# Performance work log

Hardware: AMD Instinct MI355X
Metric: run time of the kernel (lower is better)

Reference implementation:

```python
import jax, jax.numpy as jnp
import numpy as np

NEG_SLOPE = 0.2  # PyG GATConv default


def gat_layer(x, src, dst, W, att_src, att_dst, bias, num_nodes):
    """One PyG-style GATConv (concat=True, add_self_loops handled by caller).
    x: [N, F_in], W: [F_in, H*C], att_src/att_dst: [H, C], bias: [H*C].
    """
    H, C = att_src.shape
    h = (x @ W).reshape(num_nodes, H, C)              # [N, H, C]
    a_src = (h * att_src).sum(-1)                     # [N, H]
    a_dst = (h * att_dst).sum(-1)                     # [N, H]
    e = jax.nn.leaky_relu(a_src[src] + a_dst[dst], NEG_SLOPE)  # [E, H]
    # segment softmax over destination neighborhoods
    m = jax.ops.segment_max(e, dst, num_segments=num_nodes)   # [N, H]
    ex = jnp.exp(e - m[dst])
    denom = jax.ops.segment_sum(ex, dst, num_segments=num_nodes)
    alpha = ex / denom[dst]                           # [E, H]
    out = jax.ops.segment_sum(alpha[:, :, None] * h[src], dst,
                              num_segments=num_nodes)  # [N, H, C]
    return out.reshape(num_nodes, H * C) + bias


def setup_inputs() -> dict:
    key = jax.random.key(0)
    ks = jax.random.split(key, 12)
    N, E, D, H = 50000, 800000, 128, 8
    C = D // H
    x = jax.random.normal(ks[0], (N, D), dtype=jnp.float32)
    edge_index = jax.random.randint(ks[1], (2, E), 0, N, dtype=jnp.int64)
    s = 0.1
    return {
        "x": x,
        "edge_index": edge_index,
        "W1": s * jax.random.normal(ks[2], (D, H * C), dtype=jnp.float32),
        "as1": s * jax.random.normal(ks[3], (H, C), dtype=jnp.float32),
        "ad1": s * jax.random.normal(ks[4], (H, C), dtype=jnp.float32),
        "b1": jnp.zeros((H * C,), dtype=jnp.float32),
        "W2": s * jax.random.normal(ks[5], (D, H * C), dtype=jnp.float32),
        "as2": s * jax.random.normal(ks[6], (H, C), dtype=jnp.float32),
        "ad2": s * jax.random.normal(ks[7], (H, C), dtype=jnp.float32),
        "b2": jnp.zeros((H * C,), dtype=jnp.float32),
    }


def reference(x, edge_index, W1, as1, ad1, b1, W2, as2, ad2, b2):
    n = x.shape[0]
    # PyG GATConv default add_self_loops=True
    loop = jnp.arange(n, dtype=edge_index.dtype)
    src = jnp.concatenate([edge_index[0], loop])
    dst = jnp.concatenate([edge_index[1], loop])
    h = jax.nn.relu(gat_layer(x, src, dst, W1, as1, ad1, b1, n))
    # dropout p=0.5 is identity in eval mode
    return gat_layer(h, src, dst, W2, as2, ad2, b2, n)
```

## Files before the change

kernel.cpp:

```cpp
#include <hip/hip_runtime.h>
#include <math.h>

#define D 128
#define H 8
#define C 16
#define NEG_SLOPE 0.2f
#define SCAN_TILE 1024

typedef unsigned short ushortT;
typedef __attribute__((ext_vector_type(8))) short short8;
typedef __attribute__((ext_vector_type(4))) float f32x4;

__device__ __forceinline__ float bf2f(unsigned short v) {
    union { unsigned int i; float f; } c;
    c.i = ((unsigned int)v) << 16;
    return c.f;
}
__device__ __forceinline__ unsigned short f2bf(float f) {
    union { float f; unsigned int i; } c;
    c.f = f;
    unsigned int lsb = (c.i >> 16) & 1u;
    c.i += 0x7fffu + lsb;
    return (unsigned short)(c.i >> 16);
}

__device__ __forceinline__ int padc(int c) { return (c + 4) & ~3; }



__device__ __forceinline__ void hist_part(
    int tid, const int* __restrict__ ei, int* cursor, int* __restrict__ rank,
    int E) {
    int i4 = tid * 4;
    if (((E & 3) == 0) && i4 + 3 < E) {
        int4 dv = *(const int4*)(ei + (size_t)E + i4);
        int4 r;
        r.x = atomicAdd(cursor + dv.x, 1);
        r.y = atomicAdd(cursor + dv.y, 1);
        r.z = atomicAdd(cursor + dv.z, 1);
        r.w = atomicAdd(cursor + dv.w, 1);
        *(int4*)(rank + i4) = r;
    } else {
        for (int k = i4; k < E && k < i4 + 4; k++)
            rank[k] = atomicAdd(cursor + ei[(size_t)E + k], 1);
    }
}

__device__ __forceinline__ void wprep_part(
    int b2, int t, const float* __restrict__ W1, const float* __restrict__ as1,
    const float* __restrict__ ad1, const float* __restrict__ W2,
    const float* __restrict__ as2, const float* __restrict__ ad2,
    ushortT* __restrict__ wf1_hi, ushortT* __restrict__ wf1_lo,
    ushortT* __restrict__ wf2_hi, ushortT* __restrict__ wf2_lo) {
    const float *W, *att_s, *att_d;
    ushortT *whi, *wlo;
    int idx;
    if (b2 < 9) {
        W = W1; att_s = as1; att_d = ad1; whi = wf1_hi; wlo = wf1_lo;
        idx = b2 * 256 + t;
    } else {
        W = W2; att_s = as2; att_d = ad2; whi = wf2_hi; wlo = wf2_lo;
        idx = (b2 - 9) * 256 + t;
    }
    if (idx >= 4 * 9 * 64) return;
    int lane = idx & 63;
    int nt = (idx >> 6) % 9;
    int kt = idx / (9 * 64);
    int quad = lane >> 4, ncol = lane & 15;
#pragma unroll
    for (int j = 0; j < 8; j++) {
        int k = kt * 32 + quad * 8 + j;
        float v;
        if (nt < 8) {
            v = W[k * D + nt * 16 + ncol];
        } else {
            const float* att = (ncol < 8) ? att_s : att_d;
            int hd = ncol & 7;
            float s = 0.f;
            for (int c = 0; c < 16; c++)
                s += W[k * D + hd * 16 + c] * att[hd * 16 + c];
            v = s;
        }
        unsigned short hi = f2bf(v);
        unsigned short lo = f2bf(v - bf2f(hi));
        whi[idx * 8 + j] = hi;
        wlo[idx * 8 + j] = lo;
    }
}

__device__ __forceinline__ void xsplit_part(
    int idx, const float* __restrict__ x, ushortT* __restrict__ xh,
    ushortT* __restrict__ xl, int n, int nt16) {
    int r = idx >> 4;
    if (r >= nt16 * 16) return;
    int kb = idx & 15;
    float4 v0 = make_float4(0.f, 0.f, 0.f, 0.f), v1 = v0;
    if (r < n) {
        v0 = ((const float4*)(x + (size_t)r * D + kb * 8))[0];
        v1 = ((const float4*)(x + (size_t)r * D + kb * 8))[1];
    }
    int wt = r >> 4, m = r & 15, kt = kb >> 2, quad = kb & 3;
    int base = ((wt * 4 + kt) * 64 + (m + 16 * quad)) * 8;
    ushort4 h0, l0, h1, l1;
    h0.x = f2bf(v0.x); l0.x = f2bf(v0.x - bf2f(h0.x));
    h0.y = f2bf(v0.y); l0.y = f2bf(v0.y - bf2f(h0.y));
    h0.z = f2bf(v0.z); l0.z = f2bf(v0.z - bf2f(h0.z));
    h0.w = f2bf(v0.w); l0.w = f2bf(v0.w - bf2f(h0.w));
    h1.x = f2bf(v1.x); l1.x = f2bf(v1.x - bf2f(h1.x));
    h1.y = f2bf(v1.y); l1.y = f2bf(v1.y - bf2f(h1.y));
    h1.z = f2bf(v1.z); l1.z = f2bf(v1.z - bf2f(h1.z));
    h1.w = f2bf(v1.w); l1.w = f2bf(v1.w - bf2f(h1.w));
    *(ushort4*)(xh + base) = h0;
    *(ushort4*)(xh + base + 4) = h1;
    *(ushort4*)(xl + base) = l0;
    *(ushort4*)(xl + base + 4) = l1;
}

__global__ __launch_bounds__(256) void k_prep(
    const int* __restrict__ ei, int* cursor, int* __restrict__ rank, int E,
    const float* __restrict__ x, ushortT* __restrict__ xh,
    ushortT* __restrict__ xl, int n, int nt16,
    const float* __restrict__ W1, const float* __restrict__ as1,
    const float* __restrict__ ad1, const float* __restrict__ W2,
    const float* __restrict__ as2, const float* __restrict__ ad2,
    ushortT* __restrict__ wf1_hi, ushortT* __restrict__ wf1_lo,
    ushortT* __restrict__ wf2_hi, ushortT* __restrict__ wf2_lo, int nbh) {
    int b = blockIdx.x;
    int t = threadIdx.x;
    if (b < nbh) {
        hist_part(b * 256 + t, ei, cursor, rank, E);
    } else if (b < nbh + 18) {
        wprep_part(b - nbh, t, W1, as1, ad1, W2, as2, ad2,
                   wf1_hi, wf1_lo, wf2_hi, wf2_lo);
    } else {
        xsplit_part((b - nbh - 18) * 256 + t, x, xh, xl, n, nt16);
    }
}


__global__ __launch_bounds__(256) void k_scan_lb(
    const int* __restrict__ cursor, int* __restrict__ poffs,
    int* __restrict__ sstate, int* __restrict__ csrsrc, int n) {
    __shared__ int lds[256];
    __shared__ int bprefix;
    int t = threadIdx.x;
    int b = blockIdx.x;
    int base = b * SCAN_TILE + t * 4;
    int c[4] = {0, 0, 0, 0};
    if (base + 3 < n) {
        int4 q = *(const int4*)(cursor + base);
        c[0] = q.x; c[1] = q.y; c[2] = q.z; c[3] = q.w;
    } else {
        for (int k = 0; k < 4; k++)
            if (base + k < n) c[k] = cursor[base + k];
    }
    int s = padc(c[0]) + padc(c[1]) + padc(c[2]) + padc(c[3]);
    lds[t] = s;
    __syncthreads();
    for (int st = 1; st < 256; st <<= 1) {
        int add = (t >= st) ? lds[t - st] : 0;
        __syncthreads();
        lds[t] += add;
        __syncthreads();
    }
    if (t == 0)
        __hip_atomic_store(&sstate[b], lds[255] | (1 << 30),
                           __ATOMIC_RELEASE, __HIP_MEMORY_SCOPE_AGENT);
    if (t < 64) {
        int v = 0;
        if (t < b) {
            int x;
            do {
                x = __hip_atomic_load(&sstate[t], __ATOMIC_RELAXED,
                                      __HIP_MEMORY_SCOPE_AGENT);
            } while (!(x & (1 << 30)));
            v = x & 0x3FFFFFFF;
        }
#pragma unroll
        for (int o = 32; o > 0; o >>= 1) v += __shfl_down(v, o);
        if (t == 0) bprefix = v;
    }
    __syncthreads();
    int run = bprefix + ((t == 0) ? 0 : lds[t - 1]);
    if (b == 0 && t == 0) poffs[0] = 0;
#pragma unroll
    for (int k = 0; k < 4; k++) {
        int i = base + k;
        if (i < n) {
            int pv = padc(c[k]);
            csrsrc[run + c[k]] = i;
            for (int k2 = c[k] + 1; k2 < pv; k2++)
                csrsrc[run + k2] = n;
            run += pv;
            poffs[i + 1] = run;
        }
    }
}


__device__ __forceinline__ void gemm_wave(
    int wt, int lane, const ushortT* __restrict__ xh,
    const ushortT* __restrict__ xl, const ushortT* __restrict__ wf_hi,
    const ushortT* __restrict__ wf_lo, ushortT* __restrict__ hout,
    float* __restrict__ as_, float* __restrict__ ad_, int n) {
    f32x4 acc[9];
#pragma unroll
    for (int nt = 0; nt < 9; nt++) acc[nt] = (f32x4){0.f, 0.f, 0.f, 0.f};

#pragma unroll
    for (int kt = 0; kt < 4; kt++) {
        short8 a_hi = *(const short8*)(xh + (size_t)((wt * 4 + kt) * 64 + lane) * 8);
        short8 a_lo = *(const short8*)(xl + (size_t)((wt * 4 + kt) * 64 + lane) * 8);
        const ushortT* bh = wf_hi + (size_t)(kt * 576 + lane) * 8;
        const ushortT* bl = wf_lo + (size_t)(kt * 576 + lane) * 8;
#pragma unroll
        for (int nt = 0; nt < 9; nt++) {
            short8 b_hi = *(const short8*)(bh + nt * 512);
            short8 b_lo = *(const short8*)(bl + nt * 512);
            acc[nt] = __builtin_amdgcn_mfma_f32_16x16x32_bf16(a_hi, b_hi, acc[nt], 0, 0, 0);
            acc[nt] = __builtin_amdgcn_mfma_f32_16x16x32_bf16(a_lo, b_hi, acc[nt], 0, 0, 0);
            acc[nt] = __builtin_amdgcn_mfma_f32_16x16x32_bf16(a_hi, b_lo, acc[nt], 0, 0, 0);
        }
    }

    int q = lane >> 4, ncol = lane & 15;
    int rbase = wt * 16 + q * 4;
#pragma unroll
    for (int nt = 0; nt < 8; nt++) {
#pragma unroll
        for (int reg = 0; reg < 4; reg++) {
            int r = rbase + reg;
            if (r < n) hout[(size_t)r * D + nt * 16 + ncol] = f2bf(acc[nt][reg]);
        }
    }
#pragma unroll
    for (int reg = 0; reg < 4; reg++) {
        int r = rbase + reg;
        if (r < n) {
            float v = acc[8][reg];
            if (ncol < 8) as_[r * H + ncol] = v;
            else          ad_[r * H + (ncol - 8)] = v;
        }
    }
}


__global__ __launch_bounds__(256) void k_fillgemm(
    const int* __restrict__ ei, const int* __restrict__ poffs,
    const int* __restrict__ rank, int* __restrict__ csrsrc,
    ushortT* __restrict__ hbuf_s, float* __restrict__ asrc_s, int E,
    const ushortT* __restrict__ xh, const ushortT* __restrict__ xl,
    const ushortT* __restrict__ wf_hi, const ushortT* __restrict__ wf_lo,
    ushortT* __restrict__ hout, float* __restrict__ as_,
    float* __restrict__ ad_, int n, int gb) {
    int b = blockIdx.x;
    int t = threadIdx.x;
    if (b < gb) {
        int wt = b * 4 + (t >> 6);
        if (wt * 16 < n)
            gemm_wave(wt, t & 63, xh, xl, wf_hi, wf_lo, hout, as_, ad_, n);
        return;
    }
    int tid = (b - gb) * 256 + t;
    int E4 = (E + 3) >> 2;
    if (tid < E4) {
        int i4 = tid * 4;
        if (((E & 3) == 0) && i4 + 3 < E) {
            int4 sv = *(const int4*)(ei + i4);
            int4 dv = *(const int4*)(ei + (size_t)E + i4);
            int4 rv = *(const int4*)(rank + i4);
            csrsrc[poffs[dv.x] + rv.x] = sv.x;
            csrsrc[poffs[dv.y] + rv.y] = sv.y;
            csrsrc[poffs[dv.z] + rv.z] = sv.z;
            csrsrc[poffs[dv.w] + rv.w] = sv.w;
        } else {
            for (int k = i4; k < E && k < i4 + 4; k++)
                csrsrc[poffs[ei[(size_t)E + k]] + rank[k]] = ei[k];
        }
    } else if (tid == E4) {
        int total = poffs[n];
        for (int k = 0; k < 8; k++) csrsrc[total + k] = n;
        for (int k = 0; k < D; k++) hbuf_s[(size_t)n * D + k] = 0;
        for (int h = 0; h < H; h++) asrc_s[n * H + h] = -1e30f;
    }
}


__global__ __launch_bounds__(256) void k_gemm_att(
    const ushortT* __restrict__ xh, const ushortT* __restrict__ xl,
    const ushortT* __restrict__ wf_hi, const ushortT* __restrict__ wf_lo,
    ushortT* __restrict__ hout, float* __restrict__ as_,
    float* __restrict__ ad_, int n) {
    int t = threadIdx.x;
    int wt = blockIdx.x * 4 + (t >> 6);
    if (wt * 16 >= n) return;
    gemm_wave(wt, t & 63, xh, xl, wf_hi, wf_lo, hout, as_, ad_, n);
}


__global__ __launch_bounds__(256) void k_aggregate(
    const ushortT* __restrict__ hbuf, const float* __restrict__ asrc,
    const float* __restrict__ adst, const int* __restrict__ csr,
    const int* __restrict__ poffs, const float* __restrict__ bias,
    float* __restrict__ out, ushortT* __restrict__ oh, ushortT* __restrict__ ol,
    int out_mode, int n) {
    int t = threadIdx.x;
    int d = blockIdx.x * 8 + (t >> 5);
    if (d >= n) return;
    int ll = t & 31;
    int h = ll >> 2;

    int off = poffs[d];
    int degp = poffs[d + 1] - off;
    float adh = adst[d * H + h];

    float4 acc0 = make_float4(0.f, 0.f, 0.f, 0.f);
    float4 acc1 = make_float4(0.f, 0.f, 0.f, 0.f);
    float ssum = 0.f;

    int s0 = csr[off + 0], s1 = csr[off + 1], s2 = csr[off + 2], s3 = csr[off + 3];
    for (int j = 0; j < degp; j += 4) {
        int p0 = csr[off + j + 4], p1 = csr[off + j + 5];
        int p2 = csr[off + j + 6], p3 = csr[off + j + 7];
        float e0 = asrc[s0 * H + h] + adh;
        float e1 = asrc[s1 * H + h] + adh;
        float e2 = asrc[s2 * H + h] + adh;
        float e3 = asrc[s3 * H + h] + adh;
        ushort4 u0 = *(const ushort4*)(hbuf + (size_t)s0 * D + ll * 4);
        ushort4 u1 = *(const ushort4*)(hbuf + (size_t)s1 * D + ll * 4);
        ushort4 u2 = *(const ushort4*)(hbuf + (size_t)s2 * D + ll * 4);
        ushort4 u3 = *(const ushort4*)(hbuf + (size_t)s3 * D + ll * 4);
        float w0 = __expf(e0 > 0.f ? e0 : NEG_SLOPE * e0);
        float w1 = __expf(e1 > 0.f ? e1 : NEG_SLOPE * e1);
        float w2 = __expf(e2 > 0.f ? e2 : NEG_SLOPE * e2);
        float w3 = __expf(e3 > 0.f ? e3 : NEG_SLOPE * e3);
        ssum += (w0 + w1) + (w2 + w3);
        acc0.x += w0 * bf2f(u0.x); acc0.y += w0 * bf2f(u0.y);
        acc0.z += w0 * bf2f(u0.z); acc0.w += w0 * bf2f(u0.w);
        acc1.x += w1 * bf2f(u1.x); acc1.y += w1 * bf2f(u1.y);
        acc1.z += w1 * bf2f(u1.z); acc1.w += w1 * bf2f(u1.w);
        acc0.x += w2 * bf2f(u2.x); acc0.y += w2 * bf2f(u2.y);
        acc0.z += w2 * bf2f(u2.z); acc0.w += w2 * bf2f(u2.w);
        acc1.x += w3 * bf2f(u3.x); acc1.y += w3 * bf2f(u3.y);
        acc1.z += w3 * bf2f(u3.z); acc1.w += w3 * bf2f(u3.w);
        s0 = p0; s1 = p1; s2 = p2; s3 = p3;
    }

    float inv = 1.f / ssum;
    float4 b = ((const float4*)bias)[ll];
    float4 r;
    r.x = (acc0.x + acc1.x) * inv + b.x;
    r.y = (acc0.y + acc1.y) * inv + b.y;
    r.z = (acc0.z + acc1.z) * inv + b.z;
    r.w = (acc0.w + acc1.w) * inv + b.w;

    if (out_mode == 0) {
        ((float4*)(out + (size_t)d * D))[ll] = r;
    } else {
        r.x = fmaxf(r.x, 0.f);
        r.y = fmaxf(r.y, 0.f);
        r.z = fmaxf(r.z, 0.f);
        r.w = fmaxf(r.w, 0.f);
        int wt = d >> 4, m = d & 15;
        int kt = ll >> 3, quad = (ll >> 1) & 3, j0 = (ll & 1) * 4;
        int base = ((wt * 4 + kt) * 64 + (m + 16 * quad)) * 8 + j0;
        ushort4 hv, lv;
        hv.x = f2bf(r.x); lv.x = f2bf(r.x - bf2f(hv.x));
        hv.y = f2bf(r.y); lv.y = f2bf(r.y - bf2f(hv.y));
        hv.z = f2bf(r.z); lv.z = f2bf(r.z - bf2f(hv.z));
        hv.w = f2bf(r.w); lv.w = f2bf(r.w - bf2f(hv.w));
        *(ushort4*)(oh + base) = hv;
        *(ushort4*)(ol + base) = lv;
    }
}


extern "C" void kernel_launch(void* const* d_in, const int* in_sizes, int n_in,
                              void* d_out, int out_size, void* d_ws, size_t ws_size,
                              hipStream_t stream) {
    const float* x   = (const float*)d_in[0];
    const int*   ei  = (const int*)d_in[1];
    const float* W1  = (const float*)d_in[2];
    const float* as1 = (const float*)d_in[3];
    const float* ad1 = (const float*)d_in[4];
    const float* b1  = (const float*)d_in[5];
    const float* W2  = (const float*)d_in[6];
    const float* as2 = (const float*)d_in[7];
    const float* ad2 = (const float*)d_in[8];
    const float* b2  = (const float*)d_in[9];
    float* out = (float*)d_out;

    int N = in_sizes[0] / D;
    int E = in_sizes[1] / 2;
    int NT16 = (N + 15) / 16;
    int nb_scan = (N + SCAN_TILE - 1) / SCAN_TILE;
    const int WFN = 4 * 9 * 64 * 8;
    size_t XS = (size_t)NT16 * 2048;
    int E4 = (E + 3) >> 2;

    ushortT* hbuf = (ushortT*)d_ws;
    ushortT* xsh  = hbuf + (size_t)(N + 1) * D;
    ushortT* xsl  = xsh + XS;
    float* asrc = (float*)(xsl + XS);
    float* adst = asrc + (size_t)(N + 1) * H;
    int*   poffs  = (int*)(adst + (size_t)N * H);
    int*   cursor = poffs + ((N + 1 + 3) & ~3);
    int*   sstate = cursor + ((N + 3) & ~3);
    int*   rank   = sstate + 64;
    int*   csrsrc = rank + ((E + 3) & ~3);
    ushortT* wf1_hi = (ushortT*)(csrsrc + ((E + 4 * N + 8 + 3) & ~3));
    ushortT* wf1_lo = wf1_hi + WFN;
    ushortT* wf2_hi = wf1_lo + WFN;
    ushortT* wf2_lo = wf2_hi + WFN;

    hipMemsetAsync(cursor, 0, (size_t)(((N + 3) & ~3) + 64) * sizeof(int), stream);

    int nbh = (E4 + 255) / 256;
    int nbx = (NT16 * 16 * 16 + 255) / 256;
    k_prep<<<nbh + 18 + nbx, 256, 0, stream>>>(
        ei, cursor, rank, E, x, xsh, xsl, N, NT16,
        W1, as1, ad1, W2, as2, ad2, wf1_hi, wf1_lo, wf2_hi, wf2_lo, nbh);

    k_scan_lb<<<nb_scan, 256, 0, stream>>>(cursor, poffs, sstate, csrsrc, N);

    int gb = (NT16 + 3) / 4;
    int nf = (E4 + 1 + 255) / 256;
    int ab = (N + 7) / 8;
    k_fillgemm<<<gb + nf, 256, 0, stream>>>(
        ei, poffs, rank, csrsrc, hbuf, asrc, E,
        xsh, xsl, wf1_hi, wf1_lo, hbuf, asrc, adst, N, gb);
    k_aggregate<<<ab, 256, 0, stream>>>(hbuf, asrc, adst, csrsrc, poffs, b1,
                                        out, xsh, xsl, 1, N);
    k_gemm_att<<<gb, 256, 0, stream>>>(xsh, xsl, wf2_hi, wf2_lo, hbuf, asrc, adst, N);
    k_aggregate<<<ab, 256, 0, stream>>>(hbuf, asrc, adst, csrsrc, poffs, b2,
                                        out, xsh, xsl, 0, N);
}
```

Baseline: 258.5 us.

## Pad atomic counters to 64 bytes and replace stored ranks with second atomic cursor

```diff
diff --git a/kernel.cpp b/kernel.cpp
--- a/kernel.cpp
+++ b/kernel.cpp
@@ -6,6 +6,7 @@
 #define C 16
 #define NEG_SLOPE 0.2f
 #define SCAN_TILE 1024
+#define CPAD 4
 
 typedef unsigned short ushortT;
 typedef __attribute__((ext_vector_type(8))) short short8;
@@ -29,20 +30,17 @@
 
 
 __device__ __forceinline__ void hist_part(
-    int tid, const int* __restrict__ ei, int* cursor, int* __restrict__ rank,
-    int E) {
+    int tid, const int* __restrict__ ei, int* cursor, int E) {
     int i4 = tid * 4;
     if (((E & 3) == 0) && i4 + 3 < E) {
         int4 dv = *(const int4*)(ei + (size_t)E + i4);
-        int4 r;
-        r.x = atomicAdd(cursor + dv.x, 1);
-        r.y = atomicAdd(cursor + dv.y, 1);
-        r.z = atomicAdd(cursor + dv.z, 1);
-        r.w = atomicAdd(cursor + dv.w, 1);
-        *(int4*)(rank + i4) = r;
+        atomicAdd(cursor + ((size_t)dv.x << CPAD), 1);
+        atomicAdd(cursor + ((size_t)dv.y << CPAD), 1);
+        atomicAdd(cursor + ((size_t)dv.z << CPAD), 1);
+        atomicAdd(cursor + ((size_t)dv.w << CPAD), 1);
     } else {
         for (int k = i4; k < E && k < i4 + 4; k++)
-            rank[k] = atomicAdd(cursor + ei[(size_t)E + k], 1);
+            atomicAdd(cursor + ((size_t)ei[(size_t)E + k] << CPAD), 1);
     }
 }
 
@@ -117,7 +115,7 @@
 }
 
 __global__ __launch_bounds__(256) void k_prep(
-    const int* __restrict__ ei, int* cursor, int* __restrict__ rank, int E,
+    const int* __restrict__ ei, int* cursor, int E,
     const float* __restrict__ x, ushortT* __restrict__ xh,
     ushortT* __restrict__ xl, int n, int nt16,
     const float* __restrict__ W1, const float* __restrict__ as1,
@@ -128,7 +126,7 @@
     int b = blockIdx.x;
     int t = threadIdx.x;
     if (b < nbh) {
-        hist_part(b * 256 + t, ei, cursor, rank, E);
+        hist_part(b * 256 + t, ei, cursor, E);
     } else if (b < nbh + 18) {
         wprep_part(b - nbh, t, W1, as1, ad1, W2, as2, ad2,
                    wf1_hi, wf1_lo, wf2_hi, wf2_lo);
@@ -140,19 +138,18 @@
 
 __global__ __launch_bounds__(256) void k_scan_lb(
     const int* __restrict__ cursor, int* __restrict__ poffs,
-    int* __restrict__ sstate, int* __restrict__ csrsrc, int n) {
+    int* __restrict__ sstate, int* __restrict__ csrsrc,
+    int* __restrict__ curs2, int n) {
     __shared__ int lds[256];
     __shared__ int bprefix;
     int t = threadIdx.x;
     int b = blockIdx.x;
     int base = b * SCAN_TILE + t * 4;
     int c[4] = {0, 0, 0, 0};
-    if (base + 3 < n) {
-        int4 q = *(const int4*)(cursor + base);
-        c[0] = q.x; c[1] = q.y; c[2] = q.z; c[3] = q.w;
-    } else {
-        for (int k = 0; k < 4; k++)
-            if (base + k < n) c[k] = cursor[base + k];
+#pragma unroll
+    for (int k = 0; k < 4; k++) {
+        int i = base + k;
+        if (i < n) c[k] = cursor[(size_t)i << CPAD];
     }
     int s = padc(c[0]) + padc(c[1]) + padc(c[2]) + padc(c[3]);
     lds[t] = s;
@@ -188,6 +185,7 @@
         int i = base + k;
         if (i < n) {
             int pv = padc(c[k]);
+            curs2[(size_t)i << CPAD] = run;
             csrsrc[run + c[k]] = i;
             for (int k2 = c[k] + 1; k2 < pv; k2++)
                 csrsrc[run + k2] = n;
@@ -247,7 +245,7 @@
 
 __global__ __launch_bounds__(256) void k_fillgemm(
     const int* __restrict__ ei, const int* __restrict__ poffs,
-    const int* __restrict__ rank, int* __restrict__ csrsrc,
+    int* __restrict__ curs2, int* __restrict__ csrsrc,
     ushortT* __restrict__ hbuf_s, float* __restrict__ asrc_s, int E,
     const ushortT* __restrict__ xh, const ushortT* __restrict__ xl,
     const ushortT* __restrict__ wf_hi, const ushortT* __restrict__ wf_lo,
@@ -268,14 +266,19 @@
         if (((E & 3) == 0) && i4 + 3 < E) {
             int4 sv = *(const int4*)(ei + i4);
             int4 dv = *(const int4*)(ei + (size_t)E + i4);
-            int4 rv = *(const int4*)(rank + i4);
-            csrsrc[poffs[dv.x] + rv.x] = sv.x;
-            csrsrc[poffs[dv.y] + rv.y] = sv.y;
-            csrsrc[poffs[dv.z] + rv.z] = sv.z;
-            csrsrc[poffs[dv.w] + rv.w] = sv.w;
+            int r0 = atomicAdd(curs2 + ((size_t)dv.x << CPAD), 1);
+            int r1 = atomicAdd(curs2 + ((size_t)dv.y << CPAD), 1);
+            int r2 = atomicAdd(curs2 + ((size_t)dv.z << CPAD), 1);
+            int r3 = atomicAdd(curs2 + ((size_t)dv.w << CPAD), 1);
+            csrsrc[r0] = sv.x;
+            csrsrc[r1] = sv.y;
+            csrsrc[r2] = sv.z;
+            csrsrc[r3] = sv.w;
         } else {
-            for (int k = i4; k < E && k < i4 + 4; k++)
-                csrsrc[poffs[ei[(size_t)E + k]] + rank[k]] = ei[k];
+            for (int k = i4; k < E && k < i4 + 4; k++) {
+                int r = atomicAdd(curs2 + ((size_t)ei[(size_t)E + k] << CPAD), 1);
+                csrsrc[r] = ei[k];
+            }
         }
     } else if (tid == E4) {
         int total = poffs[n];
@@ -397,6 +400,7 @@
     const int WFN = 4 * 9 * 64 * 8;
     size_t XS = (size_t)NT16 * 2048;
     int E4 = (E + 3) >> 2;
+    size_t NPAD = (size_t)N << CPAD;
 
     ushortT* hbuf = (ushortT*)d_ws;
     ushortT* xsh  = hbuf + (size_t)(N + 1) * D;
@@ -405,29 +409,29 @@
     float* adst = asrc + (size_t)(N + 1) * H;
     int*   poffs  = (int*)(adst + (size_t)N * H);
     int*   cursor = poffs + ((N + 1 + 3) & ~3);
-    int*   sstate = cursor + ((N + 3) & ~3);
-    int*   rank   = sstate + 64;
-    int*   csrsrc = rank + ((E + 3) & ~3);
+    int*   sstate = cursor + NPAD;
+    int*   curs2  = sstate + 64;
+    int*   csrsrc = curs2 + NPAD;
     ushortT* wf1_hi = (ushortT*)(csrsrc + ((E + 4 * N + 8 + 3) & ~3));
     ushortT* wf1_lo = wf1_hi + WFN;
     ushortT* wf2_hi = wf1_lo + WFN;
     ushortT* wf2_lo = wf2_hi + WFN;
 
-    hipMemsetAsync(cursor, 0, (size_t)(((N + 3) & ~3) + 64) * sizeof(int), stream);
+    hipMemsetAsync(cursor, 0, (NPAD + 64) * sizeof(int), stream);
 
     int nbh = (E4 + 255) / 256;
     int nbx = (NT16 * 16 * 16 + 255) / 256;
     k_prep<<<nbh + 18 + nbx, 256, 0, stream>>>(
-        ei, cursor, rank, E, x, xsh, xsl, N, NT16,
+        ei, cursor, E, x, xsh, xsl, N, NT16,
         W1, as1, ad1, W2, as2, ad2, wf1_hi, wf1_lo, wf2_hi, wf2_lo, nbh);
 
-    k_scan_lb<<<nb_scan, 256, 0, stream>>>(cursor, poffs, sstate, csrsrc, N);
+    k_scan_lb<<<nb_scan, 256, 0, stream>>>(cursor, poffs, sstate, csrsrc, curs2, N);
 
     int gb = (NT16 + 3) / 4;
     int nf = (E4 + 1 + 255) / 256;
     int ab = (N + 7) / 8;
     k_fillgemm<<<gb + nf, 256, 0, stream>>>(
-        ei, poffs, rank, csrsrc, hbuf, asrc, E,
+        ei, poffs, curs2, csrsrc, hbuf, asrc, E,
         xsh, xsl, wf1_hi, wf1_lo, hbuf, asrc, adst, N, gb);
     k_aggregate<<<ab, 256, 0, stream>>>(hbuf, asrc, adst, csrsrc, poffs, b1,
                                         out, xsh, xsl, 1, N);
```

New measurement: 283.0 us. 1.09x slower.

## Build CSR via destination-range bucketing with LDS counting and scatter

Applied to the files above, without the earlier changes.

```diff
diff --git a/kernel.cpp b/kernel.cpp
--- a/kernel.cpp
+++ b/kernel.cpp
@@ -6,6 +6,14 @@
 #define C 16
 #define NEG_SLOPE 0.2f
 #define SCAN_TILE 1024
+
+#define BSHIFT 12
+#define BRANGE 4096
+#define NBMAX 16
+#define EPT 32
+#define BEDGES (256 * EPT)
+#define CAP 98304
+#define CSPLIT 4
 
 typedef unsigned short ushortT;
 typedef __attribute__((ext_vector_type(8))) short short8;
@@ -28,21 +36,97 @@
 
 
 
-__device__ __forceinline__ void hist_part(
-    int tid, const int* __restrict__ ei, int* cursor, int* __restrict__ rank,
-    int E) {
-    int i4 = tid * 4;
-    if (((E & 3) == 0) && i4 + 3 < E) {
-        int4 dv = *(const int4*)(ei + (size_t)E + i4);
-        int4 r;
-        r.x = atomicAdd(cursor + dv.x, 1);
-        r.y = atomicAdd(cursor + dv.y, 1);
-        r.z = atomicAdd(cursor + dv.z, 1);
-        r.w = atomicAdd(cursor + dv.w, 1);
-        *(int4*)(rank + i4) = r;
-    } else {
-        for (int k = i4; k < E && k < i4 + 4; k++)
-            rank[k] = atomicAdd(cursor + ei[(size_t)E + k], 1);
+__device__ __forceinline__ void bucket_part(
+    int b, int t, const int* __restrict__ ei, int* __restrict__ bkt,
+    int* __restrict__ bcur, int E) {
+    __shared__ int wtot[4][NBMAX];
+    __shared__ int wbase[4][NBMAX];
+    int w = t >> 6, lane = t & 63;
+    int base = b * BEDGES;
+
+    int cnt[NBMAX];
+#pragma unroll
+    for (int q = 0; q < NBMAX; q++) cnt[q] = 0;
+
+#pragma unroll
+    for (int it = 0; it < EPT / 4; it++) {
+        int idx = base + it * 1024 + t * 4;
+        if (idx + 3 < E) {
+            int4 dv = *(const int4*)(ei + (size_t)E + idx);
+            int b0 = dv.x >> BSHIFT, b1 = dv.y >> BSHIFT;
+            int b2 = dv.z >> BSHIFT, b3 = dv.w >> BSHIFT;
+#pragma unroll
+            for (int q = 0; q < NBMAX; q++)
+                cnt[q] += (b0 == q) + (b1 == q) + (b2 == q) + (b3 == q);
+        } else {
+            for (int k = idx; k < E && k < idx + 4; k++) {
+                int bq = ei[(size_t)E + k] >> BSHIFT;
+#pragma unroll
+                for (int q = 0; q < NBMAX; q++) cnt[q] += (bq == q);
+            }
+        }
+    }
+
+    int pre[NBMAX];
+#pragma unroll
+    for (int q = 0; q < NBMAX; q++) {
+        int p = cnt[q];
+#pragma unroll
+        for (int o = 1; o < 64; o <<= 1) {
+            int v = __shfl_up(p, o);
+            if (lane >= o) p += v;
+        }
+        pre[q] = p - cnt[q];
+        if (lane == 63) wtot[w][q] = p;
+    }
+    __syncthreads();
+    if (t < NBMAX) {
+        int q = t;
+        int s0 = wtot[0][q], s1 = wtot[1][q], s2 = wtot[2][q], s3 = wtot[3][q];
+        int tot = s0 + s1 + s2 + s3;
+        int gb = (tot > 0) ? atomicAdd(bcur + q * 16, tot) : 0;
+        wbase[0][q] = gb;
+        wbase[1][q] = gb + s0;
+        wbase[2][q] = gb + s0 + s1;
+        wbase[3][q] = gb + s0 + s1 + s2;
+    }
+    __syncthreads();
+    int cur[NBMAX];
+#pragma unroll
+    for (int q = 0; q < NBMAX; q++) cur[q] = wbase[w][q] + pre[q];
+
+#pragma unroll
+    for (int it = 0; it < EPT / 4; it++) {
+        int idx = base + it * 1024 + t * 4;
+        if (idx + 3 < E) {
+            int4 sv = *(const int4*)(ei + idx);
+            int4 dv = *(const int4*)(ei + (size_t)E + idx);
+            int dd[4] = {dv.x, dv.y, dv.z, dv.w};
+            int ss[4] = {sv.x, sv.y, sv.z, sv.w};
+#pragma unroll
+            for (int e = 0; e < 4; e++) {
+                int bq = dd[e] >> BSHIFT;
+                int pk = ((dd[e] & (BRANGE - 1)) << 17) | ss[e];
+                int off = cur[0];
+#pragma unroll
+                for (int q = 1; q < NBMAX; q++) off = (bq == q) ? cur[q] : off;
+                if (off < CAP) bkt[(size_t)bq * CAP + off] = pk;
+#pragma unroll
+                for (int q = 0; q < NBMAX; q++) cur[q] += (bq == q);
+            }
+        } else {
+            for (int k = idx; k < E && k < idx + 4; k++) {
+                int d = ei[(size_t)E + k], s = ei[k];
+                int bq = d >> BSHIFT;
+                int pk = ((d & (BRANGE - 1)) << 17) | s;
+                int off = cur[0];
+#pragma unroll
+                for (int q = 1; q < NBMAX; q++) off = (bq == q) ? cur[q] : off;
+                if (off < CAP) bkt[(size_t)bq * CAP + off] = pk;
+#pragma unroll
+                for (int q = 0; q < NBMAX; q++) cur[q] += (bq == q);
+            }
+        }
     }
 }
 
@@ -117,23 +201,60 @@
 }
 
 __global__ __launch_bounds__(256) void k_prep(
-    const int* __restrict__ ei, int* cursor, int* __restrict__ rank, int E,
-    const float* __restrict__ x, ushortT* __restrict__ xh,
+    const int* __restrict__ ei, int* __restrict__ bkt, int* __restrict__ bcur,
+    int E, const float* __restrict__ x, ushortT* __restrict__ xh,
     ushortT* __restrict__ xl, int n, int nt16,
     const float* __restrict__ W1, const float* __restrict__ as1,
     const float* __restrict__ ad1, const float* __restrict__ W2,
     const float* __restrict__ as2, const float* __restrict__ ad2,
     ushortT* __restrict__ wf1_hi, ushortT* __restrict__ wf1_lo,
-    ushortT* __restrict__ wf2_hi, ushortT* __restrict__ wf2_lo, int nbh) {
+    ushortT* __restrict__ wf2_hi, ushortT* __restrict__ wf2_lo, int nbb) {
     int b = blockIdx.x;
     int t = threadIdx.x;
-    if (b < nbh) {
-        hist_part(b * 256 + t, ei, cursor, rank, E);
-    } else if (b < nbh + 18) {
-        wprep_part(b - nbh, t, W1, as1, ad1, W2, as2, ad2,
+    if (b < nbb) {
+        bucket_part(b, t, ei, bkt, bcur, E);
+    } else if (b < nbb + 18) {
+        wprep_part(b - nbb, t, W1, as1, ad1, W2, as2, ad2,
                    wf1_hi, wf1_lo, wf2_hi, wf2_lo);
     } else {
-        xsplit_part((b - nbh - 18) * 256 + t, x, xh, xl, n, nt16);
+        xsplit_part((b - nbb - 18) * 256 + t, x, xh, xl, n, nt16);
+    }
+}
+
+
+__global__ __launch_bounds__(256) void k_count(
+    const int* __restrict__ bkt, const int* __restrict__ bcur,
+    int* __restrict__ cursor, int n) {
+    __shared__ int lcnt[BRANGE];
+    int t = threadIdx.x;
+    int q = blockIdx.x / CSPLIT, s = blockIdx.x % CSPLIT;
+    for (int i = t; i < BRANGE; i += 256) lcnt[i] = 0;
+    __syncthreads();
+    int tot = bcur[q * 16];
+    if (tot > CAP) tot = CAP;
+    int per = ((tot + CSPLIT - 1) / CSPLIT + 3) & ~3;
+    int lo = s * per;
+    int hi = lo + per; if (hi > tot) hi = tot;
+    const int* bp = bkt + (size_t)q * CAP;
+    for (int i = lo + t * 4; i < hi; i += 1024) {
+        if (i + 3 < hi) {
+            int4 v = *(const int4*)(bp + i);
+            atomicAdd(&lcnt[v.x >> 17], 1);
+            atomicAdd(&lcnt[v.y >> 17], 1);
+            atomicAdd(&lcnt[v.z >> 17], 1);
+            atomicAdd(&lcnt[v.w >> 17], 1);
+        } else {
+            for (int k = i; k < hi; k++) atomicAdd(&lcnt[bp[k] >> 17], 1);
+        }
+    }
+    __syncthreads();
+    int nb = q * BRANGE;
+    for (int i = t; i < BRANGE; i += 256) {
+        int node = nb + i;
+        if (node < n) {
+            int c = lcnt[i];
+            if (c) atomicAdd(&cursor[node], c);
+        }
     }
 }
 
@@ -246,13 +367,13 @@
 
 
 __global__ __launch_bounds__(256) void k_fillgemm(
-    const int* __restrict__ ei, const int* __restrict__ poffs,
-    const int* __restrict__ rank, int* __restrict__ csrsrc,
-    ushortT* __restrict__ hbuf_s, float* __restrict__ asrc_s, int E,
+    const int* __restrict__ poffs, const int* __restrict__ bkt,
+    const int* __restrict__ bcur, int* __restrict__ csrsrc,
+    ushortT* __restrict__ hbuf_s, float* __restrict__ asrc_s,
     const ushortT* __restrict__ xh, const ushortT* __restrict__ xl,
     const ushortT* __restrict__ wf_hi, const ushortT* __restrict__ wf_lo,
     ushortT* __restrict__ hout, float* __restrict__ as_,
-    float* __restrict__ ad_, int n, int gb) {
+    float* __restrict__ ad_, int n, int gb, int nbkt) {
     int b = blockIdx.x;
     int t = threadIdx.x;
     if (b < gb) {
@@ -261,23 +382,40 @@
             gemm_wave(wt, t & 63, xh, xl, wf_hi, wf_lo, hout, as_, ad_, n);
         return;
     }
-    int tid = (b - gb) * 256 + t;
-    int E4 = (E + 3) >> 2;
-    if (tid < E4) {
-        int i4 = tid * 4;
-        if (((E & 3) == 0) && i4 + 3 < E) {
-            int4 sv = *(const int4*)(ei + i4);
-            int4 dv = *(const int4*)(ei + (size_t)E + i4);
-            int4 rv = *(const int4*)(rank + i4);
-            csrsrc[poffs[dv.x] + rv.x] = sv.x;
-            csrsrc[poffs[dv.y] + rv.y] = sv.y;
-            csrsrc[poffs[dv.z] + rv.z] = sv.z;
-            csrsrc[poffs[dv.w] + rv.w] = sv.w;
-        } else {
-            for (int k = i4; k < E && k < i4 + 4; k++)
-                csrsrc[poffs[ei[(size_t)E + k]] + rank[k]] = ei[k];
-        }
-    } else if (tid == E4) {
+    int rb = b - gb;
+    if (rb < nbkt) {
+        __shared__ int cur[BRANGE];
+        int nb = rb * BRANGE;
+        for (int i = t; i < BRANGE; i += 256) {
+            int node = nb + i;
+            cur[i] = (node < n) ? poffs[node] : 0;
+        }
+        __syncthreads();
+        int tot = bcur[rb * 16];
+        if (tot > CAP) tot = CAP;
+        const int* bp = bkt + (size_t)rb * CAP;
+        for (int i = t * 4; i < tot; i += 1024) {
+            if (i + 3 < tot) {
+                int4 v = *(const int4*)(bp + i);
+                int s0 = atomicAdd(&cur[v.x >> 17], 1);
+                int s1 = atomicAdd(&cur[v.y >> 17], 1);
+                int s2 = atomicAdd(&cur[v.z >> 17], 1);
+                int s3 = atomicAdd(&cur[v.w >> 17], 1);
+                csrsrc[s0] = v.x & 0x1FFFF;
+                csrsrc[s1] = v.y & 0x1FFFF;
+                csrsrc[s2] = v.z & 0x1FFFF;
+                csrsrc[s3] = v.w & 0x1FFFF;
+            } else {
+                for (int k = i; k < tot; k++) {
+                    int v = bp[k];
+                    int s = atomicAdd(&cur[v >> 17], 1);
+                    csrsrc[s] = v & 0x1FFFF;
+                }
+            }
+        }
+        return;
+    }
+    if (rb == nbkt && t == 0) {
         int total = poffs[n];
         for (int k = 0; k < 8; k++) csrsrc[total + k] = n;
         for (int k = 0; k < D; k++) hbuf_s[(size_t)n * D + k] = 0;
@@ -394,9 +532,9 @@
     int E = in_sizes[1] / 2;
     int NT16 = (N + 15) / 16;
     int nb_scan = (N + SCAN_TILE - 1) / SCAN_TILE;
+    int nbkt = (N + BRANGE - 1) >> BSHIFT;
     const int WFN = 4 * 9 * 64 * 8;
     size_t XS = (size_t)NT16 * 2048;
-    int E4 = (E + 3) >> 2;
 
     ushortT* hbuf = (ushortT*)d_ws;
     ushortT* xsh  = hbuf + (size_t)(N + 1) * D;
@@ -406,29 +544,32 @@
     int*   poffs  = (int*)(adst + (size_t)N * H);
     int*   cursor = poffs + ((N + 1 + 3) & ~3);
     int*   sstate = cursor + ((N + 3) & ~3);
-    int*   rank   = sstate + 64;
-    int*   csrsrc = rank + ((E + 3) & ~3);
-    ushortT* wf1_hi = (ushortT*)(csrsrc + ((E + 4 * N + 8 + 3) & ~3));
+    int*   bcur   = sstate + 64;
+    int*   csrsrc = bcur + 256;
+    int*   bkt    = csrsrc + ((E + 4 * N + 8 + 3) & ~3);
+    ushortT* wf1_hi = (ushortT*)(bkt + (size_t)nbkt * CAP);
     ushortT* wf1_lo = wf1_hi + WFN;
     ushortT* wf2_hi = wf1_lo + WFN;
     ushortT* wf2_lo = wf2_hi + WFN;
 
-    hipMemsetAsync(cursor, 0, (size_t)(((N + 3) & ~3) + 64) * sizeof(int), stream);
-
-    int nbh = (E4 + 255) / 256;
+    hipMemsetAsync(cursor, 0, (size_t)(((N + 3) & ~3) + 64 + 256) * sizeof(int),
+                   stream);
+
+    int nbb = (E + BEDGES - 1) / BEDGES;
     int nbx = (NT16 * 16 * 16 + 255) / 256;
-    k_prep<<<nbh + 18 + nbx, 256, 0, stream>>>(
-        ei, cursor, rank, E, x, xsh, xsl, N, NT16,
-        W1, as1, ad1, W2, as2, ad2, wf1_hi, wf1_lo, wf2_hi, wf2_lo, nbh);
+    k_prep<<<nbb + 18 + nbx, 256, 0, stream>>>(
+        ei, bkt, bcur, E, x, xsh, xsl, N, NT16,
+        W1, as1, ad1, W2, as2, ad2, wf1_hi, wf1_lo, wf2_hi, wf2_lo, nbb);
+
+    k_count<<<nbkt * CSPLIT, 256, 0, stream>>>(bkt, bcur, cursor, N);
 
     k_scan_lb<<<nb_scan, 256, 0, stream>>>(cursor, poffs, sstate, csrsrc, N);
 
     int gb = (NT16 + 3) / 4;
-    int nf = (E4 + 1 + 255) / 256;
     int ab = (N + 7) / 8;
-    k_fillgemm<<<gb + nf, 256, 0, stream>>>(
-        ei, poffs, rank, csrsrc, hbuf, asrc, E,
-        xsh, xsl, wf1_hi, wf1_lo, hbuf, asrc, adst, N, gb);
+    k_fillgemm<<<gb + nbkt + 1, 256, 0, stream>>>(
+        poffs, bkt, bcur, csrsrc, hbuf, asrc,
+        xsh, xsl, wf1_hi, wf1_lo, hbuf, asrc, adst, N, gb, nbkt);
     k_aggregate<<<ab, 256, 0, stream>>>(hbuf, asrc, adst, csrsrc, poffs, b1,
                                         out, xsh, xsl, 1, N);
     k_gemm_att<<<gb, 256, 0, stream>>>(xsh, xsl, wf2_hi, wf2_lo, hbuf, asrc, adst, N);
```

New measurement: 299.3 us. 15.8% more time.
